# Performance work log

Hardware: AMD Instinct MI355X
Metric: run time of the kernel (lower is better)

## Reference

```python
import jax, jax.numpy as jnp
import numpy as np

B, N, C = 256, 2048, 64      # batch(residues), num_queries/keys(extra MSA seqs), channels
H, KD, VD, OD = 8, 8, 8, 64  # heads, per-head key dim, per-head value dim, output dim


def setup_inputs() -> dict:
    key = jax.random.key(0)
    ks = jax.random.split(key, 9)
    q_data = jax.random.normal(ks[0], (B, N, C), dtype=jnp.float32)
    m_data = jax.random.normal(ks[1], (B, N, C), dtype=jnp.float32)
    # per-sequence 0/1 mask, broadcast across the channel dim (same rank as q_data)
    seq_mask = (jax.random.uniform(ks[2], (B, N, 1)) < 0.9).astype(jnp.float32)
    q_mask = jnp.broadcast_to(seq_mask, (B, N, C))
    bias = jnp.zeros((B, 1, N), dtype=jnp.float32)  # ignored by forward (AF2 quirk)
    q_weights = jax.random.normal(ks[3], (C, H, KD), dtype=jnp.float32) * 0.05
    k_weights = jax.random.normal(ks[4], (C, KD), dtype=jnp.float32) * 0.05
    v_weights = jax.random.normal(ks[5], (C, VD), dtype=jnp.float32) * 0.05
    o_weights = jax.random.normal(ks[6], (H, VD, OD), dtype=jnp.float32) * 0.05
    o_bias = jnp.zeros((OD,), dtype=jnp.float32)
    gating_w = jax.random.normal(ks[7], (C, H, VD), dtype=jnp.float32) * 0.05
    gating_b = jnp.ones((H, VD), dtype=jnp.float32)
    return {
        "q_data": q_data, "m_data": m_data, "q_mask": q_mask, "bias": bias,
        "q_weights": q_weights, "k_weights": k_weights, "v_weights": v_weights,
        "o_weights": o_weights, "o_bias": o_bias,
        "gating_w": gating_w, "gating_b": gating_b,
    }


def reference(q_data, m_data, q_mask, bias, q_weights, k_weights, v_weights,
              o_weights, o_bias, gating_w, gating_b):
    # v, k projections: [B,N,C] x [C,d] -> [B,N,d]
    v = jnp.einsum('bka,ac->bkc', m_data, v_weights)
    k = jnp.einsum('bka,ac->bkc', m_data, k_weights)
    # masked mean over the query axis (dim 1); mask has full channel dim -> factor 1
    q_avg = jnp.sum(q_mask * q_data, axis=1) / (jnp.sum(q_mask, axis=1) + 1e-10)
    # pooled query: [B,C] x [C,H,KD] -> [B,H,KD], scaled by 1/sqrt(per-head key dim)
    q = jnp.einsum('ba,ahc->bhc', q_avg, q_weights) * (KD ** (-0.5))
    # attention bias from mask (the `bias` argument is overwritten, as in the original)
    mask_bias = 1e9 * (q_mask[:, None, :, 0] - 1.0)              # [B,1,N]
    logits = jnp.einsum('bhc,bkc->bhk', q, k) + mask_bias        # [B,H,N]
    weights = jax.nn.softmax(logits, axis=-1)
    weighted_avg = jnp.einsum('bhk,bkc->bhc', weights, v)        # [B,H,VD]
    # sigmoid gating per query
    gate = jax.nn.sigmoid(jnp.einsum('bqc,chv->bqhv', q_data, gating_w) + gating_b)
    gated = weighted_avg[:, None] * gate                          # [B,N,H,VD]
    out = jnp.einsum('bqhc,hco->bqo', gated, o_weights) + o_bias  # [B,N,OD]
    return out
```

## Files before the change

### kernel.cpp

```cpp
#include <hip/hip_runtime.h>
#include <hip/hip_bf16.h>
#include <math.h>

#define BN 256
#define NN 2048
#define CC 64
#define NCH 8

#define WS_SUMQ 0
#define WS_SUMM (WS_SUMQ + BN * NCH * 64)
#define WS_V    (WS_SUMM + BN * NCH)
#define WS_S    (WS_V + BN * NCH * 64)
#define WS_MASK (WS_S + BN * NCH * 8)

typedef __bf16 bf16x8 __attribute__((ext_vector_type(8)));
typedef float f32x4 __attribute__((ext_vector_type(4)));

__global__ __launch_bounds__(256) void k_pool(const float* __restrict__ qd,
                                              const float* __restrict__ qm,
                                              float* __restrict__ ws) {
    const int b = blockIdx.x >> 3, chunk = blockIdx.x & 7;
    const int tid = threadIdx.x;
    const int r = tid >> 4, c4 = tid & 15;
    const float* qb = qd + (size_t)b * NN * CC;
    const float* mb = qm + (size_t)b * NN * CC;
    float* wmask = ws + WS_MASK + (size_t)b * NN;
    const int n0 = chunk * 256;

    float4 acc = {0.f, 0.f, 0.f, 0.f};
    float msum = 0.f;
#pragma unroll
    for (int half = 0; half < 2; ++half) {
        float4 v[8];
        float m[8];
#pragma unroll
        for (int j = 0; j < 8; ++j) {
            const int n = n0 + half * 128 + j * 16 + r;
            v[j] = *(const float4*)(qb + (size_t)n * CC + c4 * 4);
            m[j] = mb[(size_t)n * CC];
        }
#pragma unroll
        for (int j = 0; j < 8; ++j) {
            acc.x += m[j] * v[j].x; acc.y += m[j] * v[j].y;
            acc.z += m[j] * v[j].z; acc.w += m[j] * v[j].w;
            msum += m[j];
            if (c4 == 0) wmask[n0 + half * 128 + j * 16 + r] = m[j];
        }
    }

    __shared__ float red[16][64];
    __shared__ float wsum[4];
    *(float4*)&red[r][c4 * 4] = acc;
    for (int off = 32; off > 0; off >>= 1) msum += __shfl_down(msum, off, 64);
    if ((tid & 63) == 0) wsum[tid >> 6] = msum;
    __syncthreads();
    if (tid < 64) {
        float s = 0.f;
#pragma unroll
        for (int rr = 0; rr < 16; ++rr) s += red[rr][tid];
        ws[WS_SUMQ + (b * 8 + chunk) * 64 + tid] = s;
    }
    if (tid == 0) {
        ws[WS_SUMM + b * 8 + chunk] =
            (wsum[0] + wsum[1] + wsum[2] + wsum[3]) * (1.f / 16.f);
    }
}

__global__ __launch_bounds__(256) void k_attn(const float* __restrict__ md,
                                              const float* __restrict__ qw,
                                              const float* __restrict__ kw,
                                              const float* __restrict__ vw,
                                              float* __restrict__ ws) {
    const int b = blockIdx.x >> 3, chunk = blockIdx.x & 7;
    const int tid = threadIdx.x;

    __shared__ float qa[64], ql[64];
    __shared__ float wkv[64][16];
    __shared__ float P[256][9];
    __shared__ float Vv[256][9];
    __shared__ float partV[4][64];
    __shared__ float partS[4][8];

    const int n = chunk * 256 + tid;
    const float* rowp = md + ((size_t)b * NN + n) * CC;
    const float mk = ws[WS_MASK + (size_t)b * NN + n];
    float4 buf[8];
#pragma unroll
    for (int j = 0; j < 8; ++j) buf[j] = ((const float4*)rowp)[j];

    if (tid < 64) {
        float s = 0.f, den = 0.f;
#pragma unroll
        for (int ch = 0; ch < 8; ++ch) {
            s += ws[WS_SUMQ + (b * 8 + ch) * 64 + tid];
            den += ws[WS_SUMM + b * 8 + ch];
        }
        qa[tid] = s / (den + 1e-10f);
    }
    __syncthreads();
    if (tid < 64) {
        float s = 0.f;
#pragma unroll
        for (int c = 0; c < 64; ++c) s += qa[c] * qw[c * 64 + tid];
        ql[tid] = s * 0.35355339059327373f;
    }
    __syncthreads();
    for (int i = tid; i < 512; i += 256) {
        const int c = i >> 3, h = i & 7;
        float s = 0.f;
#pragma unroll
        for (int d = 0; d < 8; ++d) s += kw[c * 8 + d] * ql[h * 8 + d];
        wkv[c][h] = s;
        wkv[c][8 + h] = vw[i];
    }
    __syncthreads();

    float la[8], va[8];
#pragma unroll
    for (int h = 0; h < 8; ++h) { la[h] = 0.f; va[h] = 0.f; }
#pragma unroll
    for (int half = 0; half < 2; ++half) {
        if (half == 1) {
#pragma unroll
            for (int j = 0; j < 8; ++j) buf[j] = ((const float4*)rowp)[8 + j];
        }
#pragma unroll
        for (int j = 0; j < 8; ++j) {
            const float xa[4] = {buf[j].x, buf[j].y, buf[j].z, buf[j].w};
#pragma unroll
            for (int q = 0; q < 4; ++q) {
                const int c = half * 32 + j * 4 + q;
                const float4* wr = (const float4*)wkv[c];
                const float4 wa = wr[0], wb = wr[1], wc = wr[2], wd = wr[3];
                const float x = xa[q];
                la[0] += x * wa.x; la[1] += x * wa.y; la[2] += x * wa.z; la[3] += x * wa.w;
                la[4] += x * wb.x; la[5] += x * wb.y; la[6] += x * wb.z; la[7] += x * wb.w;
                va[0] += x * wc.x; va[1] += x * wc.y; va[2] += x * wc.z; va[3] += x * wc.w;
                va[4] += x * wd.x; va[5] += x * wd.y; va[6] += x * wd.z; va[7] += x * wd.w;
            }
        }
    }

#pragma unroll
    for (int h = 0; h < 8; ++h) P[tid][h] = mk * __expf(la[h]);
#pragma unroll
    for (int d = 0; d < 8; ++d) Vv[tid][d] = va[d];
    __syncthreads();

    const int w = tid >> 6, lane = tid & 63, h = lane >> 3, d = lane & 7;
    float acc = 0.f, sacc = 0.f;
    for (int i = 0; i < 64; ++i) {
        const int rr = w * 64 + i;
        const float p = P[rr][h];
        acc += p * Vv[rr][d];
        sacc += p;
    }
    partV[w][lane] = acc;
    if (d == 0) partS[w][h] = sacc;
    __syncthreads();
    if (tid < 64)
        ws[WS_V + (b * 8 + chunk) * 64 + tid] =
            partV[0][tid] + partV[1][tid] + partV[2][tid] + partV[3][tid];
    if (tid < 8)
        ws[WS_S + (b * 8 + chunk) * 8 + tid] =
            partS[0][tid] + partS[1][tid] + partS[2][tid] + partS[3][tid];
}

__global__ __launch_bounds__(256) void k_out(const float* __restrict__ qd,
                                             const float* __restrict__ ow,
                                             const float* __restrict__ obias,
                                             const float* __restrict__ gw,
                                             const float* __restrict__ gb,
                                             const float* __restrict__ ws,
                                             float* __restrict__ out) {
    const int b = blockIdx.x >> 3, chunk = blockIdx.x & 7;
    const int tid = threadIdx.x;
    const int w = tid >> 6, lane = tid & 63, q16 = lane >> 4, c16 = lane & 15;

    __shared__ float s_wavg[64], s_sden[8];
    if (tid < 64) {
        float s = 0.f;
#pragma unroll
        for (int ch = 0; ch < 8; ++ch) s += ws[WS_V + (b * 8 + ch) * 64 + tid];
        s_wavg[tid] = s;
    }
    if (tid >= 64 && tid < 72) {
        const int hh = tid - 64;
        float s = 0.f;
#pragma unroll
        for (int ch = 0; ch < 8; ++ch) s += ws[WS_S + (b * 8 + ch) * 8 + hh];
        s_sden[hh] = s;
    }
    __syncthreads();

    bf16x8 gwf[2][4], w2f[2][4];
    float gbv[4], obv[4];
#pragma unroll
    for (int kc = 0; kc < 2; ++kc) {
        const int k0 = kc * 32 + q16 * 8;
        const float inv_s = 1.f / s_sden[k0 >> 3];
#pragma unroll
        for (int t = 0; t < 4; ++t) {
            const int n2 = t * 16 + c16;
            bf16x8 gf, wf;
#pragma unroll
            for (int j = 0; j < 8; ++j) {
                gf[j] = (__bf16)gw[(size_t)(k0 + j) * 64 + n2];
                wf[j] = (__bf16)(s_wavg[k0 + j] * inv_s *
                                 ow[(size_t)(k0 + j) * 64 + n2]);
            }
            gwf[kc][t] = gf;
            w2f[kc][t] = wf;
        }
    }
#pragma unroll
    for (int t = 0; t < 4; ++t) {
        gbv[t] = gb[t * 16 + c16];
        obv[t] = obias[t * 16 + c16];
    }

    __shared__ __align__(16) __bf16 gl[4][16][72];

    const size_t base_row = (size_t)b * NN + chunk * 256 + w * 16;

    float4 cur0, cur1, cur2, cur3, nxt0, nxt1, nxt2, nxt3;
    {
        const float* arow = qd + (base_row + c16) * CC;
        cur0 = *(const float4*)(arow + q16 * 8);
        cur1 = *(const float4*)(arow + q16 * 8 + 4);
        cur2 = *(const float4*)(arow + 32 + q16 * 8);
        cur3 = *(const float4*)(arow + 32 + q16 * 8 + 4);
    }

    for (int s = 0; s < 4; ++s) {
        if (s < 3) {
            const float* arow = qd + (base_row + (s + 1) * 64 + c16) * CC;
            nxt0 = *(const float4*)(arow + q16 * 8);
            nxt1 = *(const float4*)(arow + q16 * 8 + 4);
            nxt2 = *(const float4*)(arow + 32 + q16 * 8);
            nxt3 = *(const float4*)(arow + 32 + q16 * 8 + 4);
        }
        bf16x8 af[2];
        {
            bf16x8 a;
            a[0] = (__bf16)cur0.x; a[1] = (__bf16)cur0.y; a[2] = (__bf16)cur0.z; a[3] = (__bf16)cur0.w;
            a[4] = (__bf16)cur1.x; a[5] = (__bf16)cur1.y; a[6] = (__bf16)cur1.z; a[7] = (__bf16)cur1.w;
            af[0] = a;
            a[0] = (__bf16)cur2.x; a[1] = (__bf16)cur2.y; a[2] = (__bf16)cur2.z; a[3] = (__bf16)cur2.w;
            a[4] = (__bf16)cur3.x; a[5] = (__bf16)cur3.y; a[6] = (__bf16)cur3.z; a[7] = (__bf16)cur3.w;
            af[1] = a;
        }
        f32x4 accg[4] = {{0.f, 0.f, 0.f, 0.f}, {0.f, 0.f, 0.f, 0.f},
                         {0.f, 0.f, 0.f, 0.f}, {0.f, 0.f, 0.f, 0.f}};
#pragma unroll
        for (int kc = 0; kc < 2; ++kc)
#pragma unroll
            for (int t = 0; t < 4; ++t)
                accg[t] = __builtin_amdgcn_mfma_f32_16x16x32_bf16(af[kc], gwf[kc][t],
                                                                  accg[t], 0, 0, 0);
#pragma unroll
        for (int t = 0; t < 4; ++t)
#pragma unroll
            for (int r2 = 0; r2 < 4; ++r2) {
                const float x = accg[t][r2] + gbv[t];
                const float g = 1.f / (1.f + __expf(-x));
                gl[w][q16 * 4 + r2][t * 16 + c16] = (__bf16)g;
            }
        __asm__ volatile("s_waitcnt lgkmcnt(0)" ::: "memory");
        bf16x8 a2[2];
#pragma unroll
        for (int kc = 0; kc < 2; ++kc)
            a2[kc] = *(const bf16x8*)&gl[w][c16][kc * 32 + q16 * 8];
        f32x4 acco[4] = {{0.f, 0.f, 0.f, 0.f}, {0.f, 0.f, 0.f, 0.f},
                         {0.f, 0.f, 0.f, 0.f}, {0.f, 0.f, 0.f, 0.f}};
#pragma unroll
        for (int kc = 0; kc < 2; ++kc)
#pragma unroll
            for (int t = 0; t < 4; ++t)
                acco[t] = __builtin_amdgcn_mfma_f32_16x16x32_bf16(a2[kc], w2f[kc][t],
                                                                  acco[t], 0, 0, 0);
        __asm__ volatile("s_waitcnt lgkmcnt(0)" ::: "memory");
        float* orow = out + (base_row + s * 64) * CC;
#pragma unroll
        for (int t = 0; t < 4; ++t)
#pragma unroll
            for (int r2 = 0; r2 < 4; ++r2)
                orow[(size_t)(q16 * 4 + r2) * 64 + t * 16 + c16] = acco[t][r2] + obv[t];
        cur0 = nxt0; cur1 = nxt1; cur2 = nxt2; cur3 = nxt3;
    }
}

extern "C" void kernel_launch(void* const* d_in, const int* in_sizes, int n_in,
                              void* d_out, int out_size, void* d_ws, size_t ws_size,
                              hipStream_t stream) {
    const float* q_data = (const float*)d_in[0];
    const float* m_data = (const float*)d_in[1];
    const float* q_mask = (const float*)d_in[2];
    const float* q_w = (const float*)d_in[4];
    const float* k_w = (const float*)d_in[5];
    const float* v_w = (const float*)d_in[6];
    const float* o_w = (const float*)d_in[7];
    const float* o_b = (const float*)d_in[8];
    const float* g_w = (const float*)d_in[9];
    const float* g_b = (const float*)d_in[10];
    float* out = (float*)d_out;
    float* ws = (float*)d_ws;

    hipLaunchKernelGGL(k_pool, dim3(BN * NCH), dim3(256), 0, stream, q_data, q_mask, ws);
    hipLaunchKernelGGL(k_attn, dim3(BN * NCH), dim3(256), 0, stream, m_data, q_w, k_w,
                       v_w, ws);
    hipLaunchKernelGGL(k_out, dim3(BN * NCH), dim3(256), 0, stream, q_data, o_w, o_b,
                       g_w, g_b, ws, out);
}
```

Before: 447.9 us.

## Use 1024-thread blocks with two row-halves per batch in pool and attention kernels

The pool and attention kernels now launch 2 blocks of 1024 threads per batch row instead of 8 blocks of 256. This reduces the number of partial sums written to and re-read from workspace. The pool kernel now loads the mask once per row into shared memory and reads q_data with fully coalesced float4 indexing. The cost is larger blocks with more shared memory each (the attention kernel's 1024x17 float buffer), fewer total blocks, and wider final reductions, which may lower occupancy and latency hiding.

```diff
diff --git a/kernel.cpp b/kernel.cpp
--- a/kernel.cpp
+++ b/kernel.cpp
@@ -5,83 +5,82 @@
 #define BN 256
 #define NN 2048
 #define CC 64
-#define NCH 8
 
 #define WS_SUMQ 0
-#define WS_SUMM (WS_SUMQ + BN * NCH * 64)
-#define WS_V    (WS_SUMM + BN * NCH)
-#define WS_S    (WS_V + BN * NCH * 64)
-#define WS_MASK (WS_S + BN * NCH * 8)
+#define WS_SUMM (WS_SUMQ + BN * 2 * 64)
+#define WS_V    (WS_SUMM + BN * 2)
+#define WS_S    (WS_V + BN * 2 * 64)
+#define WS_MASK (WS_S + BN * 2 * 8)
 
 typedef __bf16 bf16x8 __attribute__((ext_vector_type(8)));
 typedef float f32x4 __attribute__((ext_vector_type(4)));
 
-__global__ __launch_bounds__(256) void k_pool(const float* __restrict__ qd,
-                                              const float* __restrict__ qm,
-                                              float* __restrict__ ws) {
-    const int b = blockIdx.x >> 3, chunk = blockIdx.x & 7;
+__global__ __launch_bounds__(1024, 8) void k_pool(const float* __restrict__ qd,
+                                                  const float* __restrict__ qm,
+                                                  float* __restrict__ ws) {
+    const int b = blockIdx.x >> 1, bh = blockIdx.x & 1;
     const int tid = threadIdx.x;
-    const int r = tid >> 4, c4 = tid & 15;
-    const float* qb = qd + (size_t)b * NN * CC;
-    const float* mb = qm + (size_t)b * NN * CC;
-    float* wmask = ws + WS_MASK + (size_t)b * NN;
-    const int n0 = chunk * 256;
-
+    const int row0 = bh * 1024;
+
+    __shared__ float smask[1024];
+    __shared__ float wsum[16];
+    __shared__ float red[64][64];
+
+    const float m0 = qm[((size_t)b * NN + row0 + tid) * CC];
+    smask[tid] = m0;
+    ws[WS_MASK + (size_t)b * NN + row0 + tid] = m0;
+    float msum = m0;
+    for (int off = 32; off > 0; off >>= 1) msum += __shfl_down(msum, off, 64);
+    if ((tid & 63) == 0) wsum[tid >> 6] = msum;
+    __syncthreads();
+
+    const float4* qb4 = (const float4*)(qd + ((size_t)b * NN + row0) * CC);
+    const int rbase = tid >> 4;
     float4 acc = {0.f, 0.f, 0.f, 0.f};
-    float msum = 0.f;
 #pragma unroll
     for (int half = 0; half < 2; ++half) {
         float4 v[8];
-        float m[8];
+#pragma unroll
+        for (int j = 0; j < 8; ++j)
+            v[j] = qb4[(size_t)(half * 8 + j) * 1024 + tid];
 #pragma unroll
         for (int j = 0; j < 8; ++j) {
-            const int n = n0 + half * 128 + j * 16 + r;
-            v[j] = *(const float4*)(qb + (size_t)n * CC + c4 * 4);
-            m[j] = mb[(size_t)n * CC];
-        }
-#pragma unroll
-        for (int j = 0; j < 8; ++j) {
-            acc.x += m[j] * v[j].x; acc.y += m[j] * v[j].y;
-            acc.z += m[j] * v[j].z; acc.w += m[j] * v[j].w;
-            msum += m[j];
-            if (c4 == 0) wmask[n0 + half * 128 + j * 16 + r] = m[j];
-        }
-    }
-
-    __shared__ float red[16][64];
-    __shared__ float wsum[4];
-    *(float4*)&red[r][c4 * 4] = acc;
-    for (int off = 32; off > 0; off >>= 1) msum += __shfl_down(msum, off, 64);
-    if ((tid & 63) == 0) wsum[tid >> 6] = msum;
-    __syncthreads();
-    if (tid < 64) {
-        float s = 0.f;
-#pragma unroll
-        for (int rr = 0; rr < 16; ++rr) s += red[rr][tid];
-        ws[WS_SUMQ + (b * 8 + chunk) * 64 + tid] = s;
+            const float m = smask[(half * 8 + j) * 64 + rbase];
+            acc.x += m * v[j].x; acc.y += m * v[j].y;
+            acc.z += m * v[j].z; acc.w += m * v[j].w;
+        }
+    }
+    *(float4*)&red[rbase][(tid & 15) * 4] = acc;
+    __syncthreads();
+    if (tid < 64) {
+        float s = 0.f;
+#pragma unroll
+        for (int g = 0; g < 64; ++g) s += red[g][tid];
+        ws[WS_SUMQ + (size_t)(b * 2 + bh) * 64 + tid] = s;
     }
     if (tid == 0) {
-        ws[WS_SUMM + b * 8 + chunk] =
-            (wsum[0] + wsum[1] + wsum[2] + wsum[3]) * (1.f / 16.f);
+        float s = 0.f;
+#pragma unroll
+        for (int g = 0; g < 16; ++g) s += wsum[g];
+        ws[WS_SUMM + b * 2 + bh] = s;
     }
 }
 
-__global__ __launch_bounds__(256) void k_attn(const float* __restrict__ md,
-                                              const float* __restrict__ qw,
-                                              const float* __restrict__ kw,
-                                              const float* __restrict__ vw,
-                                              float* __restrict__ ws) {
-    const int b = blockIdx.x >> 3, chunk = blockIdx.x & 7;
+__global__ __launch_bounds__(1024) void k_attn(const float* __restrict__ md,
+                                               const float* __restrict__ qw,
+                                               const float* __restrict__ kw,
+                                               const float* __restrict__ vw,
+                                               float* __restrict__ ws) {
+    const int b = blockIdx.x >> 1, nhalf = blockIdx.x & 1;
     const int tid = threadIdx.x;
 
     __shared__ float qa[64], ql[64];
     __shared__ float wkv[64][16];
-    __shared__ float P[256][9];
-    __shared__ float Vv[256][9];
-    __shared__ float partV[4][64];
-    __shared__ float partS[4][8];
-
-    const int n = chunk * 256 + tid;
+    __shared__ float PV[1024][17];
+    __shared__ float partV[16][64];
+    __shared__ float partS[16][8];
+
+    const int n = nhalf * 1024 + tid;
     const float* rowp = md + ((size_t)b * NN + n) * CC;
     const float mk = ws[WS_MASK + (size_t)b * NN + n];
     float4 buf[8];
@@ -89,12 +88,9 @@
     for (int j = 0; j < 8; ++j) buf[j] = ((const float4*)rowp)[j];
 
     if (tid < 64) {
-        float s = 0.f, den = 0.f;
-#pragma unroll
-        for (int ch = 0; ch < 8; ++ch) {
-            s += ws[WS_SUMQ + (b * 8 + ch) * 64 + tid];
-            den += ws[WS_SUMM + b * 8 + ch];
-        }
+        const float s = ws[WS_SUMQ + (size_t)(b * 2 + 0) * 64 + tid] +
+                        ws[WS_SUMQ + (size_t)(b * 2 + 1) * 64 + tid];
+        const float den = ws[WS_SUMM + b * 2 + 0] + ws[WS_SUMM + b * 2 + 1];
         qa[tid] = s / (den + 1e-10f);
     }
     __syncthreads();
@@ -105,13 +101,13 @@
         ql[tid] = s * 0.35355339059327373f;
     }
     __syncthreads();
-    for (int i = tid; i < 512; i += 256) {
-        const int c = i >> 3, h = i & 7;
+    if (tid < 512) {
+        const int c = tid >> 3, h = tid & 7;
         float s = 0.f;
 #pragma unroll
         for (int d = 0; d < 8; ++d) s += kw[c * 8 + d] * ql[h * 8 + d];
         wkv[c][h] = s;
-        wkv[c][8 + h] = vw[i];
+        wkv[c][8 + h] = vw[tid];
     }
     __syncthreads();
 
@@ -119,8 +115,8 @@
 #pragma unroll
     for (int h = 0; h < 8; ++h) { la[h] = 0.f; va[h] = 0.f; }
 #pragma unroll
-    for (int half = 0; half < 2; ++half) {
-        if (half == 1) {
+    for (int hv = 0; hv < 2; ++hv) {
+        if (hv == 1) {
 #pragma unroll
             for (int j = 0; j < 8; ++j) buf[j] = ((const float4*)rowp)[8 + j];
         }
@@ -129,7 +125,7 @@
             const float xa[4] = {buf[j].x, buf[j].y, buf[j].z, buf[j].w};
 #pragma unroll
             for (int q = 0; q < 4; ++q) {
-                const int c = half * 32 + j * 4 + q;
+                const int c = hv * 32 + j * 4 + q;
                 const float4* wr = (const float4*)wkv[c];
                 const float4 wa = wr[0], wb = wr[1], wc = wr[2], wd = wr[3];
                 const float x = xa[q];
@@ -142,28 +138,34 @@
     }
 
 #pragma unroll
-    for (int h = 0; h < 8; ++h) P[tid][h] = mk * __expf(la[h]);
-#pragma unroll
-    for (int d = 0; d < 8; ++d) Vv[tid][d] = va[d];
+    for (int h = 0; h < 8; ++h) PV[tid][h] = mk * __expf(la[h]);
+#pragma unroll
+    for (int d = 0; d < 8; ++d) PV[tid][8 + d] = va[d];
     __syncthreads();
 
     const int w = tid >> 6, lane = tid & 63, h = lane >> 3, d = lane & 7;
     float acc = 0.f, sacc = 0.f;
     for (int i = 0; i < 64; ++i) {
         const int rr = w * 64 + i;
-        const float p = P[rr][h];
-        acc += p * Vv[rr][d];
+        const float p = PV[rr][h];
+        acc += p * PV[rr][8 + d];
         sacc += p;
     }
     partV[w][lane] = acc;
     if (d == 0) partS[w][h] = sacc;
     __syncthreads();
-    if (tid < 64)
-        ws[WS_V + (b * 8 + chunk) * 64 + tid] =
-            partV[0][tid] + partV[1][tid] + partV[2][tid] + partV[3][tid];
-    if (tid < 8)
-        ws[WS_S + (b * 8 + chunk) * 8 + tid] =
-            partS[0][tid] + partS[1][tid] + partS[2][tid] + partS[3][tid];
+    if (tid < 64) {
+        float s = 0.f;
+#pragma unroll
+        for (int g = 0; g < 16; ++g) s += partV[g][tid];
+        ws[WS_V + (size_t)(b * 2 + nhalf) * 64 + tid] = s;
+    }
+    if (tid < 8) {
+        float s = 0.f;
+#pragma unroll
+        for (int g = 0; g < 16; ++g) s += partS[g][tid];
+        ws[WS_S + (size_t)(b * 2 + nhalf) * 8 + tid] = s;
+    }
 }
 
 __global__ __launch_bounds__(256) void k_out(const float* __restrict__ qd,
@@ -179,17 +181,13 @@
 
     __shared__ float s_wavg[64], s_sden[8];
     if (tid < 64) {
-        float s = 0.f;
-#pragma unroll
-        for (int ch = 0; ch < 8; ++ch) s += ws[WS_V + (b * 8 + ch) * 64 + tid];
-        s_wavg[tid] = s;
+        s_wavg[tid] = ws[WS_V + (size_t)(b * 2 + 0) * 64 + tid] +
+                      ws[WS_V + (size_t)(b * 2 + 1) * 64 + tid];
     }
     if (tid >= 64 && tid < 72) {
         const int hh = tid - 64;
-        float s = 0.f;
-#pragma unroll
-        for (int ch = 0; ch < 8; ++ch) s += ws[WS_S + (b * 8 + ch) * 8 + hh];
-        s_sden[hh] = s;
+        s_sden[hh] = ws[WS_S + (size_t)(b * 2 + 0) * 8 + hh] +
+                     ws[WS_S + (size_t)(b * 2 + 1) * 8 + hh];
     }
     __syncthreads();
 
@@ -306,9 +304,9 @@
     float* out = (float*)d_out;
     float* ws = (float*)d_ws;
 
-    hipLaunchKernelGGL(k_pool, dim3(BN * NCH), dim3(256), 0, stream, q_data, q_mask, ws);
-    hipLaunchKernelGGL(k_attn, dim3(BN * NCH), dim3(256), 0, stream, m_data, q_w, k_w,
+    hipLaunchKernelGGL(k_pool, dim3(BN * 2), dim3(1024), 0, stream, q_data, q_mask, ws);
+    hipLaunchKernelGGL(k_attn, dim3(BN * 2), dim3(1024), 0, stream, m_data, q_w, k_w,
                        v_w, ws);
-    hipLaunchKernelGGL(k_out, dim3(BN * NCH), dim3(256), 0, stream, q_data, o_w, o_b,
+    hipLaunchKernelGGL(k_out, dim3(BN * 8), dim3(256), 0, stream, q_data, o_w, o_b,
                        g_w, g_b, ws, out);
 }
```

After: 453.3 us. Within noise of the previous version (+1.2%).
